# Performance work log

Measured on AMD Instinct MI355X. Metric: run time of the kernel, lower is better.

The kernel has to match this reference:

```python
import jax, jax.numpy as jnp
import numpy as np

N = 50000      # nodes
E = 800000     # edges (avg degree 16)
DIN = 128      # input_dim
DG = 128       # gnn_dim
DCLS = 128     # cls_dim
DOUT = 10      # output_dim
LMDA = 1.0     # rw_lmda
P_DROP = 0.5


def setup_inputs() -> dict:
    key = jax.random.key(0)
    ks = jax.random.split(key, 12)
    x = jax.random.normal(ks[0], (N, DIN), jnp.float32)
    edge_index = jax.random.randint(ks[1], (2, E), 0, N, dtype=jnp.int64)
    edge_weight = jax.random.uniform(ks[2], (E,), jnp.float32)
    def glorot(k, shape):
        lim = np.sqrt(6.0 / (shape[0] + shape[1])).astype(np.float32)
        return jax.random.uniform(k, shape, jnp.float32, -lim, lim)
    return dict(
        x=x, edge_index=edge_index, edge_weight=edge_weight,
        W_lin_in=glorot(ks[3], (DIN, DG)), b_lin_in=jnp.zeros((DG,), jnp.float32),
        W_agg_in=glorot(ks[4], (DG + DIN, DG)), b_agg_in=jnp.zeros((DG,), jnp.float32),
        W_lin_h=glorot(ks[5], (DG, DG)), b_lin_h=jnp.zeros((DG,), jnp.float32),
        W_agg_h=glorot(ks[6], (2 * DG, DG)), b_agg_h=jnp.zeros((DG,), jnp.float32),
        W_mlp1=glorot(ks[7], (DG, DCLS)), b_mlp1=jnp.zeros((DCLS,), jnp.float32),
        W_mlp2=glorot(ks[8], (DCLS, DOUT)), b_mlp2=jnp.zeros((DOUT,), jnp.float32),
    )


def _gs_layer(x, row, col, ew, inv_cnt, W_lin, b_lin, W_agg, b_agg):
    # GS_reweight: message = (1-lmda)*lin(x_j) + lmda*ew*lin(x_j), mean-aggregated
    # at row (flow='target_to_source': gather from col, scatter to row).
    h = x @ W_lin + b_lin                      # [N, DG] (lin before gather == lin(x_j))
    hj = h[col]                                # [E, DG] gather
    m = (1.0 - LMDA) * hj + LMDA * (ew[:, None] * hj)
    agg = jax.ops.segment_sum(m, row, num_segments=N) * inv_cnt[:, None]  # mean
    out = jnp.concatenate([agg, x], axis=-1) @ W_agg + b_agg              # update()
    return jax.nn.relu(out)


def _dropout(x, k):
    mask = jax.random.bernoulli(k, 1.0 - P_DROP, x.shape)
    return jnp.where(mask, x / (1.0 - P_DROP), 0.0)


def reference(x, edge_index, edge_weight,
              W_lin_in, b_lin_in, W_agg_in, b_agg_in,
              W_lin_h, b_lin_h, W_agg_h, b_agg_h,
              W_mlp1, b_mlp1, W_mlp2, b_mlp2):
    row, col = edge_index[0], edge_index[1]
    cnt = jax.ops.segment_sum(jnp.ones((E,), x.dtype), row, num_segments=N)
    inv_cnt = 1.0 / jnp.maximum(cnt, 1.0)     # scatter_mean: empty rows -> 0
    dk = jax.random.split(jax.random.key(42), 3)
    h = _gs_layer(x, row, col, edge_weight, inv_cnt, W_lin_in, b_lin_in, W_agg_in, b_agg_in)
    h = _dropout(jax.nn.relu(h), dk[0])       # relu is idempotent after update's relu
    for i in range(2):                        # layers 2,3 share prop_hidden weights
        h = _gs_layer(h, row, col, edge_weight, inv_cnt, W_lin_h, b_lin_h, W_agg_h, b_agg_h)
        h = _dropout(jax.nn.relu(h), dk[i + 1])
    y = jax.nn.relu(h @ W_mlp1 + b_mlp1) @ W_mlp2 + b_mlp2  # cls_layers=2, bn=False
    return (h, y)
```

## Files before the change

kernel.cpp:

```cpp
#include <hip/hip_runtime.h>
#include <cstdint>
#include <cstddef>


#define N_NODES 50000
#define N_EDGES 800000
#define DGN 128
#define DOUT 10
#define NELEM (N_NODES * DGN)
#define NMASKW (NELEM / 64)
#define NBINS 391
#define TILE 4096
#define BSTR 4096
#define NTILES ((N_EDGES + TILE - 1) / TILE)
#define GBF ((N_NODES + 63) / 64)
#define MK_BLOCKS 25000

#define XB_BLK 6250
#define HI_BLK NTILES
#define WC_BLK 128
#define TR_BLK 192
#define R0 XB_BLK
#define R1 (R0 + HI_BLK)
#define R2 (R1 + WC_BLK)
#define R3 (R2 + TR_BLK)
#define MEGA_BLOCKS (R3 + 1)

#define AB_BLOCKS ((N_NODES + 3) / 4)

typedef __attribute__((ext_vector_type(8))) short bf16x8;
typedef __attribute__((ext_vector_type(4))) float f32x4;

__host__ __device__ static inline unsigned short f2bf(float f) {
  union { float f; unsigned u; } c; c.f = f;
  unsigned u = c.u;
  return (unsigned short)((u + 0x7fffu + ((u >> 16) & 1u)) >> 16);
}
__device__ static inline float bflo(unsigned u) { return __uint_as_float(u << 16); }
__device__ static inline float bfhi(unsigned u) { return __uint_as_float(u & 0xffff0000u); }
__device__ static inline float bf2f(unsigned short h) {
  return __uint_as_float(((unsigned)h) << 16);
}

__host__ __device__ static inline void tf2x32(unsigned k0, unsigned k1,
                                              unsigned c0, unsigned c1,
                                              unsigned& o0, unsigned& o1) {
  unsigned ks2 = k0 ^ k1 ^ 0x1BD11BDAu;
  unsigned x0 = c0 + k0;
  unsigned x1 = c1 + k1;
#define TFR(r) { x0 += x1; x1 = (x1 << (r)) | (x1 >> (32 - (r))); x1 ^= x0; }
  TFR(13) TFR(15) TFR(26) TFR(6)
  x0 += k1;  x1 += ks2 + 1u;
  TFR(17) TFR(29) TFR(16) TFR(24)
  x0 += ks2; x1 += k0 + 2u;
  TFR(13) TFR(15) TFR(26) TFR(6)
  x0 += k0;  x1 += k1 + 3u;
  TFR(17) TFR(29) TFR(16) TFR(24)
  x0 += k1;  x1 += ks2 + 4u;
  TFR(13) TFR(15) TFR(26) TFR(6)
  x0 += ks2; x1 += k0 + 5u;
#undef TFR
  o0 = x0; o1 = x1;
}

__device__ static inline void mask_chunk(unsigned long long* __restrict__ gm,
                                         int i, unsigned k0, unsigned k1) {
  unsigned o0, o1;
  tf2x32(k0, k1, 0u, (unsigned)i, o0, o1);
  unsigned long long b = __ballot(((o0 ^ o1) >> 31) == 0u);
  if ((threadIdx.x & 63) == 0) gm[i >> 6] = b;
}

__global__ __launch_bounds__(256) void mega_kernel(
    const float* __restrict__ x, unsigned short* __restrict__ xb,
    const int* __restrict__ ei, int* __restrict__ chist,
    const float* __restrict__ Wli, const float* __restrict__ Wai,
    const float* __restrict__ Wlh, const float* __restrict__ Wah,
    const float* __restrict__ Wm1,
    const float* __restrict__ bli, const float* __restrict__ blh,
    unsigned short* __restrict__ Tai, unsigned short* __restrict__ Tah,
    unsigned short* __restrict__ Tm1,
    float* __restrict__ bvi, float* __restrict__ bvh) {
  __shared__ int h[NBINS];
  const int b = blockIdx.x;
  const int tid = threadIdx.x;

  if (b < R0) {
    int g = b * 256 + tid;
    float4 v = ((const float4*)x)[g];
    ushort4 o;
    o.x = f2bf(v.x); o.y = f2bf(v.y); o.z = f2bf(v.z); o.w = f2bf(v.w);
    ((ushort4*)xb)[g] = o;
  } else if (b < R1) {
    for (int i = tid; i < NBINS; i += 256) h[i] = 0;
    __syncthreads();
    const int e0 = (b - R0) * TILE;
#pragma unroll 4
    for (int j = 0; j < TILE; j += 256) {
      int e = e0 + j + tid;
      if (e < N_EDGES) {
        int r = ei[e];
        r = (r < 0) ? 0 : (r >= N_NODES ? N_NODES - 1 : r);
        atomicAdd(&h[r >> 7], 1);
      }
    }
    __syncthreads();
    for (int i = tid; i < NBINS; i += 256)
      if (h[i]) atomicAdd(&chist[i], h[i]);
  } else if (b < R2) {
    int idx = (b - R1) * 256 + tid;
    int n = idx & 127;
    int k = (idx >> 7) & 127;
    int m = idx >> 14;
    const float* Wl = m ? Wlh : Wli;
    const float* Wa = m ? Wah : Wai;
    unsigned short* T = m ? Tah : Tai;
    float acc = 0.0f;
#pragma unroll 8
    for (int j = 0; j < 128; ++j)
      acc += Wl[k * 128 + j] * Wa[j * 128 + n];
    T[n * 256 + k] = f2bf(acc);
  } else if (b < R3) {
    int j = (b - R2) * 256 + tid;
    if (j < 16384) {
      int kk = j & 127, n = j >> 7;
      Tai[n * 256 + 128 + kk] = f2bf(Wai[(size_t)(128 + kk) * 128 + n]);
    } else if (j < 32768) {
      int q = j - 16384;
      int kk = q & 127, n = q >> 7;
      Tah[n * 256 + 128 + kk] = f2bf(Wah[(size_t)(128 + kk) * 128 + n]);
    } else {
      int q = j - 32768;
      int k = q & 127, n = q >> 7;
      Tm1[n * 128 + k] = f2bf(Wm1[(size_t)k * 128 + n]);
    }
  } else {
    int n = tid & 127;
    const float* bl = (tid < 128) ? bli : blh;
    const float* Wa = (tid < 128) ? Wai : Wah;
    float acc = 0.0f;
    for (int j = 0; j < 128; ++j) acc += bl[j] * Wa[j * 128 + n];
    if (tid < 128) bvi[n] = acc; else bvh[n] = acc;
  }
}

__global__ __launch_bounds__(256) void scatter_kernel(const int* __restrict__ ei,
                                                      const float* __restrict__ ew,
                                                      int* __restrict__ ccursor,
                                                      uint2* __restrict__ pk) {
  __shared__ uint2 st[TILE];
  __shared__ unsigned short sbin[TILE];
  __shared__ int h[NBINS];
  __shared__ int base[NBINS];
  __shared__ int gbase[NBINS];
  __shared__ int cur[NBINS];
  __shared__ int sc[512];
  const int tid = threadIdx.x;
  const int e0 = blockIdx.x * TILE;
  const int nt = (N_EDGES - e0 < TILE) ? (N_EDGES - e0) : TILE;

  for (int i = tid; i < NBINS; i += 256) { h[i] = 0; cur[i] = 0; }
  __syncthreads();
  for (int j = tid; j < nt; j += 256) {
    int r = ei[e0 + j];
    r = (r < 0) ? 0 : (r >= N_NODES ? N_NODES - 1 : r);
    atomicAdd(&h[r >> 7], 1);
  }
  __syncthreads();
  sc[tid] = (tid < NBINS) ? h[tid] : 0;
  sc[tid + 256] = (tid + 256 < NBINS) ? h[tid + 256] : 0;
  __syncthreads();
  for (int off = 1; off < 512; off <<= 1) {
    int a0 = (tid >= off) ? sc[tid - off] : 0;
    int a1 = (tid + 256 >= off) ? sc[tid + 256 - off] : 0;
    __syncthreads();
    sc[tid] += a0; sc[tid + 256] += a1;
    __syncthreads();
  }
  if (tid < NBINS) {
    base[tid] = sc[tid] - h[tid];
    if (h[tid]) gbase[tid] = tid * BSTR + atomicAdd(&ccursor[tid], h[tid]);
  }
  if (tid + 256 < NBINS) {
    base[tid + 256] = sc[tid + 256] - h[tid + 256];
    if (h[tid + 256])
      gbase[tid + 256] = (tid + 256) * BSTR + atomicAdd(&ccursor[tid + 256], h[tid + 256]);
  }
  __syncthreads();
  for (int j = tid; j < nt; j += 256) {
    int r = ei[e0 + j];
    r = (r < 0) ? 0 : (r >= N_NODES ? N_NODES - 1 : r);
    int c = ei[N_EDGES + e0 + j];
    c = (c < 0) ? 0 : (c >= N_NODES ? N_NODES - 1 : c);
    int bb = r >> 7;
    int slot = base[bb] + atomicAdd(&cur[bb], 1);
    uint2 p;
    p.x = ((unsigned)r << 16) | (unsigned)c;
    p.y = __float_as_uint(ew[e0 + j]);
    st[slot] = p;
    sbin[slot] = (unsigned short)bb;
  }
  __syncthreads();
  for (int j = tid; j < nt; j += 256) {
    int bb = sbin[j];
    pk[(size_t)gbase[bb] + (j - base[bb])] = st[j];
  }
}

__global__ __launch_bounds__(256) void place_kernel(const int* __restrict__ chist,
                                                    const uint2* __restrict__ pk,
                                                    uint2* __restrict__ csr,
                                                    int* __restrict__ rowptr,
                                                    float* __restrict__ invc) {
  __shared__ int red[256];
  __shared__ int lcnt[128];
  __shared__ int lpre[128];
  __shared__ int lcur[128];
  __shared__ int sc[128];
  const int b = blockIdx.x;
  const int tid = threadIdx.x;

  int psum = 0;
  for (int i = tid; i < b; i += 256) psum += chist[i];
  red[tid] = psum;
  __syncthreads();
  for (int off = 128; off > 0; off >>= 1) {
    if (tid < off) red[tid] += red[tid + off];
    __syncthreads();
  }
  const int cb = red[0];
  const int n = chist[b];
  const uint2* __restrict__ pkb = pk + (size_t)b * BSTR;
  const int r0 = b << 7;
  const int nr = (N_NODES - r0 < 128) ? (N_NODES - r0) : 128;

  if (tid < 128) { lcnt[tid] = 0; lcur[tid] = 0; }
  __syncthreads();
  for (int i = tid; i < n; i += 256) {
    int r7 = (int)(pkb[i].x >> 16) - r0;
    atomicAdd(&lcnt[r7], 1);
  }
  __syncthreads();
  if (tid < 128) sc[tid] = lcnt[tid];
  __syncthreads();
  for (int off = 1; off < 128; off <<= 1) {
    int tv = (tid >= off && tid < 128) ? sc[tid - off] : 0;
    __syncthreads();
    if (tid < 128) sc[tid] += tv;
    __syncthreads();
  }
  if (tid < 128) lpre[tid] = sc[tid] - lcnt[tid];
  __syncthreads();
  if (tid < nr) {
    rowptr[r0 + tid] = cb + lpre[tid];
    int c = lcnt[tid];
    invc[r0 + tid] = 1.0f / (float)(c > 1 ? c : 1);
  }
  if (b == NBINS - 1 && tid == 0) rowptr[N_NODES] = N_EDGES;
  for (int i = tid; i < n; i += 256) {
    uint2 p = pkb[i];
    int r7 = (int)(p.x >> 16) - r0;
    int slot = cb + lpre[r7] + atomicAdd(&lcur[r7], 1);
    uint2 o;
    o.x = p.x & 0xFFFFu;
    o.y = p.y;
    csr[slot] = o;
  }
}

__global__ __launch_bounds__(256) void agg_kernel(const unsigned short* __restrict__ hlin,
                                                  const int* __restrict__ rowptr,
                                                  const uint2* __restrict__ csr,
                                                  const float* __restrict__ invc,
                                                  unsigned short* __restrict__ agg,
                                                  float* __restrict__ swout,
                                                  unsigned long long* __restrict__ gm,
                                                  unsigned gk0, unsigned gk1) {
  if (blockIdx.x >= AB_BLOCKS) {
    mask_chunk(gm, (blockIdx.x - AB_BLOCKS) * 256 + threadIdx.x, gk0, gk1);
    return;
  }
  const int r = blockIdx.x * 4 + (threadIdx.x >> 6);
  const int lane = threadIdx.x & 63;
  const int es = lane >> 4;
  const int cg = lane & 15;
  const int start = rowptr[r];
  const int num = rowptr[r + 1] - start;
  const uint4* __restrict__ H = (const uint4*)hlin;

  int qi = (num > 0) ? (start + (lane < num ? lane : num - 1)) : 0;
  uint2 myq = csr[qi];

  float a[8] = {0.f, 0.f, 0.f, 0.f, 0.f, 0.f, 0.f, 0.f};
  float ws = 0.f;
  const int nb = (num < 64) ? num : 64;
  for (int e = 0; e < nb; e += 16) {
#pragma unroll
    for (int j = 0; j < 4; ++j) {
      int idx = e + j * 4 + es;
      bool ok = idx < nb;
      int sl = ok ? idx : nb - 1;
      int c0 = __shfl((int)myq.x, sl);
      int w0 = __shfl((int)myq.y, sl);
      unsigned col = (unsigned)c0;
      float w = ok ? __uint_as_float((unsigned)w0) : 0.0f;
      uint4 p = H[(size_t)col * 16 + cg];
      ws += w;
      a[0] += w * bflo(p.x); a[1] += w * bfhi(p.x);
      a[2] += w * bflo(p.y); a[3] += w * bfhi(p.y);
      a[4] += w * bflo(p.z); a[5] += w * bfhi(p.z);
      a[6] += w * bflo(p.w); a[7] += w * bfhi(p.w);
    }
  }
  for (int e = 64; e < num; e += 16) {
#pragma unroll
    for (int j = 0; j < 4; ++j) {
      int idx = e + j * 4 + es;
      bool ok = idx < num;
      int idxc = ok ? idx : (num - 1);
      uint2 q = csr[start + idxc];
      float w = ok ? __uint_as_float(q.y) : 0.0f;
      uint4 p = H[(size_t)q.x * 16 + cg];
      ws += w;
      a[0] += w * bflo(p.x); a[1] += w * bfhi(p.x);
      a[2] += w * bflo(p.y); a[3] += w * bfhi(p.y);
      a[4] += w * bflo(p.z); a[5] += w * bfhi(p.z);
      a[6] += w * bflo(p.w); a[7] += w * bfhi(p.w);
    }
  }
#pragma unroll
  for (int k = 0; k < 8; ++k) {
    a[k] += __shfl_xor(a[k], 32);
    a[k] += __shfl_xor(a[k], 16);
  }
  ws += __shfl_xor(ws, 32);
  ws += __shfl_xor(ws, 16);
  const float s = invc[r];
  if (es == 0) {
    uint4 o;
    o.x = (unsigned)f2bf(a[0] * s) | ((unsigned)f2bf(a[1] * s) << 16);
    o.y = (unsigned)f2bf(a[2] * s) | ((unsigned)f2bf(a[3] * s) << 16);
    o.z = (unsigned)f2bf(a[4] * s) | ((unsigned)f2bf(a[5] * s) << 16);
    o.w = (unsigned)f2bf(a[6] * s) | ((unsigned)f2bf(a[7] * s) << 16);
    ((uint4*)agg)[(size_t)r * 16 + cg] = o;
  }
  if (swout && lane == 0) swout[r] = ws * s;
}

template <bool WF32, bool MLP>
__global__ __launch_bounds__(256) void layer_gemm(
    const unsigned short* __restrict__ Agg, const unsigned short* __restrict__ Hin,
    const unsigned short* __restrict__ Wt,
    const float* __restrict__ bvec, const float* __restrict__ bagg,
    const float* __restrict__ sw,
    const unsigned long long* __restrict__ maskw,
    float* __restrict__ outf, unsigned short* __restrict__ outb,
    const unsigned short* __restrict__ Wt2,
    const float* __restrict__ b1,
    const float* __restrict__ W2, const float* __restrict__ b2,
    float* __restrict__ y) {
  constexpr int LS = 72;
  constexpr int LT = 132;
  __shared__ unsigned short Als[64 * LS];
  __shared__ unsigned short Bls[128 * LS];
  __shared__ unsigned short tT[MLP ? 64 * LT : 2];
  __shared__ float Ws[MLP ? 128 * DOUT : 1];
  __shared__ float bs[MLP ? DOUT : 1];
  const int tid = threadIdx.x;
  const int m0 = blockIdx.x * 64;
  const int lane = tid & 63;
  const int wid = tid >> 6;
  const int wm = (wid >> 1) * 32;
  const int wn = (wid & 1) * 64;
  const int ln = lane & 15;
  const int lh = lane >> 4;
  const int sArow = tid >> 2;
  const int sAk = (tid & 3) * 16;
  const int sBcol = tid >> 1;
  const int sBk = (tid & 1) * 32;
  int arow = m0 + sArow;
  if (arow >= N_NODES) arow = N_NODES - 1;

  if (MLP) {
    for (int i = tid; i < 128 * DOUT; i += 256) Ws[i] = W2[i];
    if (tid < DOUT) bs[tid] = b2[tid];
  }

  f32x4 acc[2][4];
#pragma unroll
  for (int i = 0; i < 2; ++i)
#pragma unroll
    for (int j = 0; j < 4; ++j)
#pragma unroll
      for (int r = 0; r < 4; ++r) acc[i][j][r] = 0.0f;

  for (int kb = 0; kb < 256; kb += 64) {
    const unsigned short* Asrc = (kb < 128) ? Agg : Hin;
    const unsigned short* ap = Asrc + (size_t)arow * 128 + (kb & 127) + sAk;
    unsigned short* al = &Als[sArow * LS + sAk];
    *(uint4*)(al + 0) = *(const uint4*)(ap + 0);
    *(uint4*)(al + 8) = *(const uint4*)(ap + 8);
    const unsigned short* bp = Wt + (size_t)sBcol * 256 + kb + sBk;
    unsigned short* bl = &Bls[sBcol * LS + sBk];
    *(uint4*)(bl + 0)  = *(const uint4*)(bp + 0);
    *(uint4*)(bl + 8)  = *(const uint4*)(bp + 8);
    *(uint4*)(bl + 16) = *(const uint4*)(bp + 16);
    *(uint4*)(bl + 24) = *(const uint4*)(bp + 24);
    __syncthreads();
#pragma unroll
    for (int ks = 0; ks < 64; ks += 32) {
      bf16x8 af[2], bfr[4];
#pragma unroll
      for (int i = 0; i < 2; ++i)
        af[i] = *(const bf16x8*)&Als[(wm + i * 16 + ln) * LS + ks + lh * 8];
#pragma unroll
      for (int j = 0; j < 4; ++j)
        bfr[j] = *(const bf16x8*)&Bls[(wn + j * 16 + ln) * LS + ks + lh * 8];
#pragma unroll
      for (int i = 0; i < 2; ++i)
#pragma unroll
        for (int j = 0; j < 4; ++j)
          acc[i][j] = __builtin_amdgcn_mfma_f32_16x16x32_bf16(af[i], bfr[j], acc[i][j], 0, 0, 0);
    }
    __syncthreads();
  }

  const int lm = lane >> 4;
  float bc[4], b2c[4];
#pragma unroll
  for (int j = 0; j < 4; ++j) {
    int col = wn + j * 16 + ln;
    bc[j] = bvec[col];
    b2c[j] = bagg[col];
  }
#pragma unroll
  for (int i = 0; i < 2; ++i) {
    const int lr0 = wm + i * 16 + lm * 4;
#pragma unroll
    for (int r = 0; r < 4; ++r) {
      const int row = m0 + lr0 + r;
      if (row >= N_NODES) continue;
      const float swr = sw[row];
      const unsigned long long mw = maskw[(size_t)row * 2 + (wn >> 6)];
#pragma unroll
      for (int j = 0; j < 4; ++j) {
        const int col = wn + j * 16 + ln;
        float v = acc[i][j][r] + swr * bc[j] + b2c[j];
        v = fmaxf(v, 0.0f);
        v = ((mw >> (col & 63)) & 1ull) ? 2.0f * v : 0.0f;
        if (WF32) outf[(size_t)row * DGN + col] = v;
        if (MLP) tT[(lr0 + r) * LT + col] = f2bf(v);
        else outb[(size_t)row * DGN + col] = f2bf(v);
      }
    }
  }

  if (MLP) {
    __syncthreads();

    f32x4 acc2[2][4];
#pragma unroll
    for (int i = 0; i < 2; ++i)
#pragma unroll
      for (int j = 0; j < 4; ++j)
#pragma unroll
        for (int r = 0; r < 4; ++r) acc2[i][j][r] = 0.0f;

    for (int kb = 0; kb < 128; kb += 64) {
      const unsigned short* bp = Wt2 + (size_t)sBcol * 128 + kb + sBk;
      unsigned short* bl = &Bls[sBcol * LS + sBk];
      *(uint4*)(bl + 0)  = *(const uint4*)(bp + 0);
      *(uint4*)(bl + 8)  = *(const uint4*)(bp + 8);
      *(uint4*)(bl + 16) = *(const uint4*)(bp + 16);
      *(uint4*)(bl + 24) = *(const uint4*)(bp + 24);
      __syncthreads();
#pragma unroll
      for (int ks = 0; ks < 64; ks += 32) {
        bf16x8 af[2], bfr[4];
#pragma unroll
        for (int i = 0; i < 2; ++i)
          af[i] = *(const bf16x8*)&tT[(wm + i * 16 + ln) * LT + kb + ks + lh * 8];
#pragma unroll
        for (int j = 0; j < 4; ++j)
          bfr[j] = *(const bf16x8*)&Bls[(wn + j * 16 + ln) * LS + ks + lh * 8];
#pragma unroll
        for (int i = 0; i < 2; ++i)
#pragma unroll
          for (int j = 0; j < 4; ++j)
            acc2[i][j] = __builtin_amdgcn_mfma_f32_16x16x32_bf16(af[i], bfr[j], acc2[i][j], 0, 0, 0);
      }
      __syncthreads();
    }

    float bcol[4];
#pragma unroll
    for (int j = 0; j < 4; ++j) bcol[j] = b1[wn + j * 16 + ln];
#pragma unroll
    for (int i = 0; i < 2; ++i) {
      const int lr0 = wm + i * 16 + lm * 4;
#pragma unroll
      for (int r = 0; r < 4; ++r) {
        const int lr = lr0 + r;
#pragma unroll
        for (int j = 0; j < 4; ++j) {
          const int col = wn + j * 16 + ln;
          float v = fmaxf(acc2[i][j][r] + bcol[j], 0.0f);
          tT[lr * LT + col] = f2bf(v);
        }
      }
    }
    __syncthreads();

    if (tid < 64) {
      int row = m0 + tid;
      if (row < N_NODES) {
        float a2[DOUT];
#pragma unroll
        for (int c = 0; c < DOUT; ++c) a2[c] = bs[c];
        const unsigned short* tr = &tT[tid * LT];
#pragma unroll 8
        for (int k = 0; k < 128; ++k) {
          float tv = bf2f(tr[k]);
          const float* wr = &Ws[k * DOUT];
#pragma unroll
          for (int c = 0; c < DOUT; ++c) a2[c] += tv * wr[c];
        }
        float* yp = y + (size_t)row * DOUT;
#pragma unroll
        for (int c = 0; c < DOUT; ++c) yp[c] = a2[c];
      }
    }
  }
}

extern "C" void kernel_launch(void* const* d_in, const int* in_sizes, int n_in,
                              void* d_out, int out_size, void* d_ws, size_t ws_size,
                              hipStream_t stream) {
  const float* x        = (const float*)d_in[0];
  const int*   ei       = (const int*)d_in[1];
  const float* ew       = (const float*)d_in[2];
  const float* W_lin_in = (const float*)d_in[3];
  const float* b_lin_in = (const float*)d_in[4];
  const float* W_agg_in = (const float*)d_in[5];
  const float* b_agg_in = (const float*)d_in[6];
  const float* W_lin_h  = (const float*)d_in[7];
  const float* b_lin_h  = (const float*)d_in[8];
  const float* W_agg_h  = (const float*)d_in[9];
  const float* b_agg_h  = (const float*)d_in[10];
  const float* W_mlp1   = (const float*)d_in[11];
  const float* b_mlp1   = (const float*)d_in[12];
  const float* W_mlp2   = (const float*)d_in[13];
  const float* b_mlp2   = (const float*)d_in[14];

  float* hout = (float*)d_out;
  float* yout = hout + (size_t)NELEM;

  char* p = (char*)d_ws;
  auto alloc = [&](size_t bytes) {
    char* q = p;
    p += (bytes + 255) & ~(size_t)255;
    return q;
  };
  int*   chist   = (int*)alloc((size_t)(NBINS + 1) * 4);
  int*   ccursor = (int*)alloc((size_t)NBINS * 4);
  int*   rowptr  = (int*)alloc((size_t)(N_NODES + 1) * 4);
  float* invc    = (float*)alloc((size_t)N_NODES * 4);
  float* swv     = (float*)alloc((size_t)N_NODES * 4);
  uint2* pk      = (uint2*)alloc((size_t)NBINS * BSTR * 8);
  uint2* csr     = (uint2*)alloc((size_t)N_EDGES * 8);
  unsigned short* xb   = (unsigned short*)alloc((size_t)NELEM * 2);
  unsigned short* aggb = (unsigned short*)alloc((size_t)NELEM * 2);
  unsigned short* hA   = (unsigned short*)alloc((size_t)NELEM * 2);
  unsigned short* hB   = (unsigned short*)alloc((size_t)NELEM * 2);
  unsigned long long* mw0 = (unsigned long long*)alloc((size_t)NMASKW * 8);
  unsigned long long* mw1 = (unsigned long long*)alloc((size_t)NMASKW * 8);
  unsigned long long* mw2 = (unsigned long long*)alloc((size_t)NMASKW * 8);
  unsigned short* Tai = (unsigned short*)alloc(32768 * 2);
  unsigned short* Tah = (unsigned short*)alloc(32768 * 2);
  unsigned short* Tm1 = (unsigned short*)alloc(16384 * 2);
  float* bvi = (float*)alloc(128 * 4);
  float* bvh = (float*)alloc(128 * 4);

  unsigned dk[3][2];
  for (unsigned i = 0; i < 3; ++i) tf2x32(0u, 42u, 0u, i, dk[i][0], dk[i][1]);

  hipMemsetAsync(chist, 0, (size_t)(NBINS + 1) * 4, stream);
  hipMemsetAsync(ccursor, 0, (size_t)NBINS * 4, stream);
  mega_kernel<<<MEGA_BLOCKS, 256, 0, stream>>>(
      x, xb, ei, chist, W_lin_in, W_agg_in, W_lin_h, W_agg_h, W_mlp1,
      b_lin_in, b_lin_h, Tai, Tah, Tm1, bvi, bvh);

  scatter_kernel<<<NTILES, 256, 0, stream>>>(ei, ew, ccursor, pk);
  place_kernel<<<NBINS, 256, 0, stream>>>(chist, pk, csr, rowptr, invc);

  agg_kernel<<<AB_BLOCKS + MK_BLOCKS, 256, 0, stream>>>(
      xb, rowptr, csr, invc, aggb, swv, mw0, dk[0][0], dk[0][1]);
  layer_gemm<false, false><<<GBF, 256, 0, stream>>>(
      aggb, xb, Tai, bvi, b_agg_in, swv, mw0, nullptr, hA,
      nullptr, nullptr, nullptr, nullptr, nullptr);

  agg_kernel<<<AB_BLOCKS + MK_BLOCKS, 256, 0, stream>>>(
      hA, rowptr, csr, invc, aggb, nullptr, mw1, dk[1][0], dk[1][1]);
  layer_gemm<false, false><<<GBF, 256, 0, stream>>>(
      aggb, hA, Tah, bvh, b_agg_h, swv, mw1, nullptr, hB,
      nullptr, nullptr, nullptr, nullptr, nullptr);

  agg_kernel<<<AB_BLOCKS + MK_BLOCKS, 256, 0, stream>>>(
      hB, rowptr, csr, invc, aggb, nullptr, mw2, dk[2][0], dk[2][1]);
  layer_gemm<true, true><<<GBF, 256, 0, stream>>>(
      aggb, hB, Tah, bvh, b_agg_h, swv, mw2, hout, nullptr,
      Tm1, b_mlp1, W_mlp2, b_mlp2, yout);
}
```

Before: 328.1 us.

## Move dropout mask generation from agg kernels into scatter and GEMM kernels

Dropout mask generation blocks are no longer appended to each aggregation launch. Mask 0 is now built by extra blocks in the scatter kernel, and masks 1 and 2 by extra blocks in the preceding layer GEMM launches. The aim is to take compute-bound RNG work off the latency-sensitive gather kernels and overlap it with the lower-occupancy GEMM and scatter launches. The cost is that shared-memory-heavy kernels get many trivial extra blocks, which may contend with the main blocks.

```diff
diff --git a/kernel.cpp b/kernel.cpp
--- a/kernel.cpp
+++ b/kernel.cpp
@@ -147,7 +147,13 @@
 __global__ __launch_bounds__(256) void scatter_kernel(const int* __restrict__ ei,
                                                       const float* __restrict__ ew,
                                                       int* __restrict__ ccursor,
-                                                      uint2* __restrict__ pk) {
+                                                      uint2* __restrict__ pk,
+                                                      unsigned long long* __restrict__ mg0,
+                                                      unsigned k00, unsigned k01) {
+  if (blockIdx.x >= NTILES) {
+    mask_chunk(mg0, (blockIdx.x - NTILES) * 256 + threadIdx.x, k00, k01);
+    return;
+  }
   __shared__ uint2 st[TILE];
   __shared__ unsigned short sbin[TILE];
   __shared__ int h[NBINS];
@@ -273,13 +279,7 @@
                                                   const uint2* __restrict__ csr,
                                                   const float* __restrict__ invc,
                                                   unsigned short* __restrict__ agg,
-                                                  float* __restrict__ swout,
-                                                  unsigned long long* __restrict__ gm,
-                                                  unsigned gk0, unsigned gk1) {
-  if (blockIdx.x >= AB_BLOCKS) {
-    mask_chunk(gm, (blockIdx.x - AB_BLOCKS) * 256 + threadIdx.x, gk0, gk1);
-    return;
-  }
+                                                  float* __restrict__ swout) {
   const int r = blockIdx.x * 4 + (threadIdx.x >> 6);
   const int lane = threadIdx.x & 63;
   const int es = lane >> 4;
@@ -347,7 +347,7 @@
   if (swout && lane == 0) swout[r] = ws * s;
 }
 
-template <bool WF32, bool MLP>
+template <bool WF32, bool MASKGEN, bool MLP>
 __global__ __launch_bounds__(256) void layer_gemm(
     const unsigned short* __restrict__ Agg, const unsigned short* __restrict__ Hin,
     const unsigned short* __restrict__ Wt,
@@ -355,10 +355,15 @@
     const float* __restrict__ sw,
     const unsigned long long* __restrict__ maskw,
     float* __restrict__ outf, unsigned short* __restrict__ outb,
+    unsigned long long* __restrict__ gm, unsigned gk0, unsigned gk1,
     const unsigned short* __restrict__ Wt2,
     const float* __restrict__ b1,
     const float* __restrict__ W2, const float* __restrict__ b2,
     float* __restrict__ y) {
+  if (MASKGEN && blockIdx.x >= GBF) {
+    mask_chunk(gm, (blockIdx.x - GBF) * 256 + threadIdx.x, gk0, gk1);
+    return;
+  }
   constexpr int LS = 72;
   constexpr int LT = 132;
   __shared__ unsigned short Als[64 * LS];
@@ -590,24 +595,22 @@
       x, xb, ei, chist, W_lin_in, W_agg_in, W_lin_h, W_agg_h, W_mlp1,
       b_lin_in, b_lin_h, Tai, Tah, Tm1, bvi, bvh);
 
-  scatter_kernel<<<NTILES, 256, 0, stream>>>(ei, ew, ccursor, pk);
+  scatter_kernel<<<NTILES + MK_BLOCKS, 256, 0, stream>>>(
+      ei, ew, ccursor, pk, mw0, dk[0][0], dk[0][1]);
   place_kernel<<<NBINS, 256, 0, stream>>>(chist, pk, csr, rowptr, invc);
 
-  agg_kernel<<<AB_BLOCKS + MK_BLOCKS, 256, 0, stream>>>(
-      xb, rowptr, csr, invc, aggb, swv, mw0, dk[0][0], dk[0][1]);
-  layer_gemm<false, false><<<GBF, 256, 0, stream>>>(
+  agg_kernel<<<AB_BLOCKS, 256, 0, stream>>>(xb, rowptr, csr, invc, aggb, swv);
+  layer_gemm<false, true, false><<<GBF + MK_BLOCKS, 256, 0, stream>>>(
       aggb, xb, Tai, bvi, b_agg_in, swv, mw0, nullptr, hA,
-      nullptr, nullptr, nullptr, nullptr, nullptr);
-
-  agg_kernel<<<AB_BLOCKS + MK_BLOCKS, 256, 0, stream>>>(
-      hA, rowptr, csr, invc, aggb, nullptr, mw1, dk[1][0], dk[1][1]);
-  layer_gemm<false, false><<<GBF, 256, 0, stream>>>(
+      mw1, dk[1][0], dk[1][1], nullptr, nullptr, nullptr, nullptr, nullptr);
+
+  agg_kernel<<<AB_BLOCKS, 256, 0, stream>>>(hA, rowptr, csr, invc, aggb, nullptr);
+  layer_gemm<false, true, false><<<GBF + MK_BLOCKS, 256, 0, stream>>>(
       aggb, hA, Tah, bvh, b_agg_h, swv, mw1, nullptr, hB,
-      nullptr, nullptr, nullptr, nullptr, nullptr);
-
-  agg_kernel<<<AB_BLOCKS + MK_BLOCKS, 256, 0, stream>>>(
-      hB, rowptr, csr, invc, aggb, nullptr, mw2, dk[2][0], dk[2][1]);
-  layer_gemm<true, true><<<GBF, 256, 0, stream>>>(
+      mw2, dk[2][0], dk[2][1], nullptr, nullptr, nullptr, nullptr, nullptr);
+
+  agg_kernel<<<AB_BLOCKS, 256, 0, stream>>>(hB, rowptr, csr, invc, aggb, nullptr);
+  layer_gemm<true, false, true><<<GBF, 256, 0, stream>>>(
       aggb, hB, Tah, bvh, b_agg_h, swv, mw2, hout, nullptr,
-      Tm1, b_mlp1, W_mlp2, b_mlp2, yout);
-}
+      nullptr, 0, 0, Tm1, b_mlp1, W_mlp2, b_mlp2, yout);
+}
```

After: 310.0 us. -5.5%, faster.
